# Kernel optimization log

Hardware: AMD Instinct MI355X
Metric: run time of the kernel (lower is better)

The kernel has to match this reference:

```python
import jax, jax.numpy as jnp
import numpy as np

B, N, F, K, NK, MID = 64, 100, 2048, 16, 8, 1024


def setup_inputs() -> dict:
    key = jax.random.key(0)
    ks = jax.random.split(key, 10)
    v = jax.random.normal(ks[0], (B, N, F), dtype=jnp.float32)
    v_mask = jnp.ones((B, N), dtype=jnp.float32)
    coord = jax.random.normal(ks[1], (B, N, N, 2), dtype=jnp.float32)
    adj_matrix = jax.random.uniform(ks[2], (B, N, K), dtype=jnp.float32)
    top_ind = jax.random.randint(ks[3], (B, N, K), 0, N)
    mean_rho = jax.random.uniform(ks[4], (NK,), minval=0.0, maxval=1.0)
    mean_theta = jax.random.uniform(ks[5], (NK,), minval=-np.pi, maxval=np.pi)
    precision_rho = jax.random.uniform(ks[6], (NK,), minval=0.0, maxval=1.0)
    precision_theta = jax.random.uniform(ks[7], (NK,), minval=0.0, maxval=1.0)
    # stacked per-kernel Linear weights: [NK, MID//NK, F] (no bias)
    W = jax.random.normal(ks[8], (NK, MID // NK, F), dtype=jnp.float32) * 0.02
    return {"v": v, "v_mask": v_mask, "coord": coord, "adj_matrix": adj_matrix,
            "top_ind": top_ind, "mean_rho": mean_rho, "mean_theta": mean_theta,
            "precision_rho": precision_rho, "precision_theta": precision_theta, "W": W}


def _gaussian_weights(coord, mean_rho, mean_theta, precision_rho, precision_theta):
    # coord: [B, N, N, 2] -> weights [B, N, N, NK], normalized over kernel axis
    rho = coord[..., 0][..., None]    # [B,N,N,1]
    theta = coord[..., 1][..., None]  # [B,N,N,1]
    w_rho = jnp.exp(-0.5 * (rho - mean_rho) ** 2 / (1e-14 + precision_rho ** 2))
    first_angle = jnp.abs(theta - mean_theta)
    second_angle = jnp.abs(2.0 * np.pi - first_angle)
    w_theta = jnp.exp(-0.5 * jnp.minimum(first_angle, second_angle) ** 2
                      / (1e-14 + precision_theta ** 2))
    w = w_rho * w_theta
    w = jnp.where(jnp.isnan(w), 0.0, w)
    # torch code normalizes the (-1, NK) view over dim=1 == kernel axis
    return w / (jnp.sum(w, axis=-1, keepdims=True) + 1e-14)


def reference(v, v_mask, coord, adj_matrix, top_ind,
              mean_rho, mean_theta, precision_rho, precision_theta, W):
    coord_weight = _gaussian_weights(coord, mean_rho, mean_theta,
                                     precision_rho, precision_theta)  # [B,N,N,NK]
    # gather top-K neighbor features: sparse_v[b,i,k] = v[b, top_ind[b,i,k]]
    sparse_v = jax.vmap(lambda vb, idx: vb[idx])(v, top_ind)           # [B,N,K,F]
    # gather corresponding Gaussian weights along neighbor axis
    sparse_weight = jnp.take_along_axis(coord_weight, top_ind[..., None], axis=2)  # [B,N,K,NK]
    attentive_v = sparse_v * adj_matrix[..., None]                     # weight_adj=True
    # weighted_neighbourhood = sparse_weight^T @ attentive_v : [B,N,NK,F]
    wn = jnp.einsum('bnkm,bnkf->bnmf', sparse_weight, attentive_v)
    # per-kernel linear then concat over kernels -> [B,N,NK*(MID//NK)]
    out = jnp.einsum('bnmf,mof->bnmo', wn, W)
    return out.reshape(v.shape[0], v.shape[1], -1)
```

## Files before the change

kernel.cpp:

```cpp
#include <hip/hip_runtime.h>
#include <math.h>

#define Bc 64
#define Nc 100
#define Fc 2048
#define Kc 16
#define NKc 8
#define BN (Bc*Nc)
#define MO 1024
#define TWO_PI 6.283185307179586f

typedef __attribute__((ext_vector_type(8))) short bf16x8;
typedef __attribute__((ext_vector_type(4))) float f32x4;

__device__ __forceinline__ unsigned short f2bf(float x) {
    union { float f; unsigned u; } c; c.f = x;
    unsigned r = c.u + 0x7FFFu + ((c.u >> 16) & 1u);
    return (unsigned short)(r >> 16);
}
__device__ __forceinline__ float bf2f(unsigned short x) {
    return __uint_as_float((unsigned)x << 16);
}

__global__ __launch_bounds__(256) void cvt_both(
    const float* __restrict__ v, const float* __restrict__ W,
    unsigned short* __restrict__ dst, int n8v, int n8tot)
{
    for (int i = blockIdx.x * blockDim.x + threadIdx.x; i < n8tot;
         i += gridDim.x * blockDim.x) {
        const float* src = (i < n8v) ? (v + (size_t)i * 8)
                                     : (W + (size_t)(i - n8v) * 8);
        const float4 x0 = ((const float4*)src)[0];
        const float4 x1 = ((const float4*)src)[1];
        bf16x8 o;
        o[0]=(short)f2bf(x0.x); o[1]=(short)f2bf(x0.y);
        o[2]=(short)f2bf(x0.z); o[3]=(short)f2bf(x0.w);
        o[4]=(short)f2bf(x1.x); o[5]=(short)f2bf(x1.y);
        o[6]=(short)f2bf(x1.z); o[7]=(short)f2bf(x1.w);
        *(bf16x8*)(dst + (size_t)i * 8) = o;
    }
}

__global__ __launch_bounds__(128) void weights_k(
    const float* __restrict__ coord, const float* __restrict__ adj,
    const int* __restrict__ top_ind,
    const float* __restrict__ mean_rho, const float* __restrict__ mean_theta,
    const float* __restrict__ prec_rho, const float* __restrict__ prec_theta,
    float* __restrict__ aw)
{
    __shared__ int   idx[Kc];
    __shared__ float wv[Kc][NKc];
    __shared__ float sc[Kc];
    const int bn = blockIdx.x;
    const int tid = threadIdx.x;
    if (tid < Kc) idx[tid] = top_ind[bn * Kc + tid];
    __syncthreads();
    const int k = tid >> 3, m = tid & 7;
    const int j = idx[k];
    const float rho   = coord[((size_t)bn * Nc + j) * 2 + 0];
    const float theta = coord[((size_t)bn * Nc + j) * 2 + 1];
    const float dr = rho - mean_rho[m];
    const float pr = prec_rho[m];
    const float wr = expf(-0.5f * dr * dr / (1e-14f + pr * pr));
    const float fa = fabsf(theta - mean_theta[m]);
    const float sa = fabsf(TWO_PI - fa);
    const float da = fminf(fa, sa);
    const float pt = prec_theta[m];
    const float wt = expf(-0.5f * da * da / (1e-14f + pt * pt));
    float w = wr * wt;
    if (w != w) w = 0.0f;
    wv[k][m] = w;
    __syncthreads();
    if (tid < Kc) {
        float s = 0.f;
        #pragma unroll
        for (int mm = 0; mm < NKc; ++mm) s += wv[tid][mm];
        sc[tid] = adj[bn * Kc + tid] / (s + 1e-14f);
    }
    __syncthreads();
    aw[(size_t)bn * 128 + m * 16 + k] = wv[k][m] * sc[k];
}

#define GBM 112
#define GBN 128
#define GBK 64
#define NT (Fc/GBK)
#define A_OFF   0
#define A_BUF   14336
#define B_OFF   28672
#define B_BUF   16384
#define IDX_OFF 30720
#define AW_OFF  37120

#define SYNC() do { asm volatile("s_waitcnt vmcnt(0)" ::: "memory"); \
                    __builtin_amdgcn_s_barrier(); \
                    __builtin_amdgcn_sched_barrier(0); } while (0)

template<int MI>
__device__ __forceinline__ void compute_tile(
    f32x4 (&acc)[4][4], const unsigned char* smem,
    int buf, int wm, int wn, int fr, int kg, int rsw)
{
    #pragma unroll
    for (int kk = 0; kk < 2; ++kk) {
        bf16x8 af[MI], bfr[4];
        #pragma unroll
        for (int mi = 0; mi < MI; ++mi)
            af[mi] = *(const bf16x8*)(smem + A_OFF + buf * A_BUF
                        + (wm * 64 + mi * 16 + fr) * 128
                        + ((kk * 32 + kg) ^ rsw) * 2);
        #pragma unroll
        for (int ni = 0; ni < 4; ++ni)
            bfr[ni] = *(const bf16x8*)(smem + B_OFF + buf * B_BUF
                        + (wn * 64 + ni * 16 + fr) * 128
                        + ((kk * 32 + kg) ^ rsw) * 2);
        #pragma unroll
        for (int mi = 0; mi < MI; ++mi)
            #pragma unroll
            for (int ni = 0; ni < 4; ++ni)
                acc[mi][ni] = __builtin_amdgcn_mfma_f32_16x16x32_bf16(
                    af[mi], bfr[ni], acc[mi][ni], 0, 0, 0);
    }
}

__global__ __launch_bounds__(256) void gemm_fused(
    const unsigned short* __restrict__ A,
    const unsigned short* __restrict__ B,
    const float* __restrict__ aw,
    const int* __restrict__ top_ind,
    float* __restrict__ out)
{
    __shared__ __align__(16) unsigned char smem[61440];

    const int tid = threadIdx.x;
    const int w  = tid >> 6, l = tid & 63;
    const int wm = w & 1,  wn = w >> 1;
    const int bid = blockIdx.x;
    const int b  = bid >> 3;
    const int jt = bid & 7;
    const int i0 = b * Nc;
    const int j0 = jt * GBN;

    const int srow = tid >> 3;
    const int scol = 8 * ((l & 7) ^ (l >> 3));

    const int fr = l & 15;
    const int kg = (l >> 4) * 8;
    const int rsw = 8 * (fr & 7);

    f32x4 acc[4][4] = {};

    auto stage = [&](int buf, int t) {
        const size_t k0 = (size_t)t * GBK;
        #pragma unroll
        for (int q = 0; q < 4; ++q) {
            const int row = q * 32 + srow;
            __builtin_amdgcn_global_load_lds(
                (const __attribute__((address_space(1))) void*)
                    (B + (size_t)(j0 + row) * Fc + k0 + scol),
                (__attribute__((address_space(3))) void*)
                    (smem + B_OFF + buf * B_BUF + q * 4096 + w * 1024),
                16, 0, 0);
        }
        #pragma unroll
        for (int q = 0; q < 3; ++q) {
            const int row = i0 + q * 32 + srow;
            __builtin_amdgcn_global_load_lds(
                (const __attribute__((address_space(1))) void*)
                    (A + (size_t)row * Fc + k0 + scol),
                (__attribute__((address_space(3))) void*)
                    (smem + A_OFF + buf * A_BUF + q * 4096 + w * 1024),
                16, 0, 0);
        }
        if (tid < 128) {
            int row = i0 + 96 + srow;
            if (row > BN - 1) row = BN - 1;
            __builtin_amdgcn_global_load_lds(
                (const __attribute__((address_space(1))) void*)
                    (A + (size_t)row * Fc + k0 + scol),
                (__attribute__((address_space(3))) void*)
                    (smem + A_OFF + buf * A_BUF + 3 * 4096 + w * 1024),
                16, 0, 0);
        }
    };

    #define COMPUTE(buf) do { \
        if (wm == 0) compute_tile<4>(acc, smem, (buf), wm, wn, fr, kg, rsw); \
        else         compute_tile<3>(acc, smem, (buf), wm, wn, fr, kg, rsw); \
    } while (0)

    stage(0, 0);
    SYNC();
    int t = 0;
    for (; t + 2 < NT; t += 2) {
        stage(1, t + 1);  COMPUTE(0);  SYNC();
        stage(0, t + 2);  COMPUTE(1);  SYNC();
    }
    stage(1, NT - 1);  COMPUTE(0);  SYNC();
    COMPUTE(1);

    __syncthreads();
    const int cn = l & 15;
    const int cr = (l >> 4) * 4;
    const int MIw = 4 - wm;
    #pragma unroll
    for (int mi = 0; mi < 4; ++mi) {
        if (mi < MIw) {
            #pragma unroll
            for (int ni = 0; ni < 4; ++ni) {
                #pragma unroll
                for (int r = 0; r < 4; ++r) {
                    const int row = wm * 64 + mi * 16 + cr + r;
                    const int col = wn * 64 + ni * 16 + cn;
                    *(unsigned short*)(smem + row * 264 + col * 2) =
                        f2bf(acc[mi][ni][r]);
                }
            }
        }
    }
    for (int i = tid; i < Nc * Kc; i += 256) {
        ((int*)(smem + IDX_OFF))[i] = top_ind[(size_t)b * Nc * Kc + i];
        ((float*)(smem + AW_OFF))[i] =
            aw[(size_t)(b * Nc + (i >> 4)) * 128 + jt * 16 + (i & 15)];
    }
    __syncthreads();

    const int cq = tid & 31;
    for (int n = tid >> 5; n < Nc; n += 8) {
        float4 o = make_float4(0.f, 0.f, 0.f, 0.f);
        #pragma unroll
        for (int k = 0; k < Kc; ++k) {
            const int   r = ((const int*)(smem + IDX_OFF))[n * Kc + k];
            const float a = ((const float*)(smem + AW_OFF))[n * Kc + k];
            const ushort4 u = *(const ushort4*)(smem + r * 264 + cq * 8);
            o.x += a * bf2f(u.x); o.y += a * bf2f(u.y);
            o.z += a * bf2f(u.z); o.w += a * bf2f(u.w);
        }
        *(float4*)&out[(size_t)(b * Nc + n) * MO + j0 + cq * 4] = o;
    }
}

#define TM 64
#define TN 64
#define FBK 16

__device__ __forceinline__ void compute_a(
    int bn, int tid,
    const float* __restrict__ coord, const float* __restrict__ adj,
    const int* __restrict__ top_ind,
    const float* __restrict__ mean_rho, const float* __restrict__ mean_theta,
    const float* __restrict__ prec_rho, const float* __restrict__ prec_theta,
    int (&lds_idx)[Kc], float (&lds_a)[Kc][NKc], float (&lds_scale)[Kc])
{
    if (tid < Kc) lds_idx[tid] = top_ind[bn * Kc + tid];
    __syncthreads();
    if (tid < Kc * NKc) {
        const int k = tid >> 3, m = tid & 7;
        const int j = lds_idx[k];
        const float rho   = coord[((size_t)bn * Nc + j) * 2 + 0];
        const float theta = coord[((size_t)bn * Nc + j) * 2 + 1];
        const float dr = rho - mean_rho[m];
        const float pr = prec_rho[m];
        const float wr = expf(-0.5f * dr * dr / (1e-14f + pr * pr));
        const float fa = fabsf(theta - mean_theta[m]);
        const float sa = fabsf(TWO_PI - fa);
        const float da = fminf(fa, sa);
        const float pt = prec_theta[m];
        const float wt = expf(-0.5f * da * da / (1e-14f + pt * pt));
        float w = wr * wt;
        if (w != w) w = 0.0f;
        lds_a[k][m] = w;
    }
    __syncthreads();
    if (tid < Kc) {
        float s = 0.f;
        #pragma unroll
        for (int m = 0; m < NKc; ++m) s += lds_a[tid][m];
        lds_scale[tid] = adj[bn * Kc + tid] / (s + 1e-14f);
    }
    __syncthreads();
    if (tid < Kc * NKc) {
        const int k = tid >> 3, m = tid & 7;
        lds_a[k][m] *= lds_scale[k];
    }
    __syncthreads();
}

__global__ __launch_bounds__(256) void gemm_p(
    const float* __restrict__ A,
    const float* __restrict__ Bm,
    float* __restrict__ P)
{
    __shared__ float At[FBK][TM + 4];
    __shared__ float Bt[FBK][TN + 4];
    const int tid = threadIdx.x;
    const int tx = tid & 15;
    const int ty = tid >> 4;
    const int i0 = blockIdx.x * TM;
    const int j0 = blockIdx.y * TN;
    const int lk = tid & 15;
    const int lr = tid >> 4;

    float acc[4][4] = {};

    for (int k0 = 0; k0 < Fc; k0 += FBK) {
        #pragma unroll
        for (int rr = 0; rr < 4; ++rr) {
            At[lk][lr + rr * 16] = A[(size_t)(i0 + lr + rr * 16) * Fc + k0 + lk];
            Bt[lk][lr + rr * 16] = Bm[(size_t)(j0 + lr + rr * 16) * Fc + k0 + lk];
        }
        __syncthreads();
        #pragma unroll
        for (int kk = 0; kk < FBK; ++kk) {
            float a4[4], b4[4];
            #pragma unroll
            for (int p = 0; p < 4; ++p) a4[p] = At[kk][ty * 4 + p];
            #pragma unroll
            for (int p = 0; p < 4; ++p) b4[p] = Bt[kk][tx * 4 + p];
            #pragma unroll
            for (int pi = 0; pi < 4; ++pi)
                #pragma unroll
                for (int pj = 0; pj < 4; ++pj)
                    acc[pi][pj] += a4[pi] * b4[pj];
        }
        __syncthreads();
    }

    #pragma unroll
    for (int pi = 0; pi < 4; ++pi)
        #pragma unroll
        for (int pj = 0; pj < 4; ++pj)
            P[(size_t)(i0 + ty * 4 + pi) * MO + j0 + tx * 4 + pj] = acc[pi][pj];
}

__global__ __launch_bounds__(256) void combine_f32(
    const float* __restrict__ P,
    const float* __restrict__ coord, const float* __restrict__ adj,
    const int* __restrict__ top_ind,
    const float* __restrict__ mr, const float* __restrict__ mt,
    const float* __restrict__ pr, const float* __restrict__ pt,
    float* __restrict__ out)
{
    __shared__ int   lds_idx[Kc];
    __shared__ float lds_a[Kc][NKc];
    __shared__ float lds_scale[Kc];
    const int bn = blockIdx.x;
    const int tid = threadIdx.x;
    const int b = bn / Nc;

    compute_a(bn, tid, coord, adj, top_ind, mr, mt, pr, pt,
              lds_idx, lds_a, lds_scale);

    const int m = tid >> 5;
    float ak[Kc];
    size_t rowoff[Kc];
    #pragma unroll
    for (int k = 0; k < Kc; ++k) {
        ak[k] = lds_a[k][m];
        rowoff[k] = (size_t)(b * Nc + lds_idx[k]) * MO + tid * 4;
    }
    float4 acc = make_float4(0.f, 0.f, 0.f, 0.f);
    #pragma unroll
    for (int k = 0; k < Kc; ++k) {
        const float4 p = *(const float4*)&P[rowoff[k]];
        acc.x += ak[k] * p.x; acc.y += ak[k] * p.y;
        acc.z += ak[k] * p.z; acc.w += ak[k] * p.w;
    }
    *(float4*)&out[(size_t)bn * MO + tid * 4] = acc;
}

extern "C" void kernel_launch(void* const* d_in, const int* in_sizes, int n_in,
                              void* d_out, int out_size, void* d_ws, size_t ws_size,
                              hipStream_t stream) {
    const float* v        = (const float*)d_in[0];
    const float* coord    = (const float*)d_in[2];
    const float* adj      = (const float*)d_in[3];
    const int*   top_ind  = (const int*)d_in[4];
    const float* mr       = (const float*)d_in[5];
    const float* mt       = (const float*)d_in[6];
    const float* pr       = (const float*)d_in[7];
    const float* pt       = (const float*)d_in[8];
    const float* W        = (const float*)d_in[9];
    float* out = (float*)d_out;

    const size_t vbBytes = (size_t)BN * Fc * sizeof(unsigned short);
    const size_t WbBytes = (size_t)MO * Fc * sizeof(unsigned short);
    const size_t awBytes = (size_t)BN * 128 * sizeof(float);
    const size_t needBF  = vbBytes + WbBytes + awBytes;
    const size_t PBytes  = (size_t)BN * MO * sizeof(float);

    if (ws_size >= needBF) {
        char* ws = (char*)d_ws;
        unsigned short* vb = (unsigned short*)ws;
        unsigned short* Wb = vb + (size_t)BN * Fc;
        float* aw          = (float*)(ws + vbBytes + WbBytes);

        const int n8v   = BN * Fc / 8;
        const int n8tot = n8v + MO * Fc / 8;
        cvt_both<<<7424, 256, 0, stream>>>(v, W, vb, n8v, n8tot);

        weights_k<<<BN, 128, 0, stream>>>(coord, adj, top_ind,
                                          mr, mt, pr, pt, aw);

        gemm_fused<<<512, 256, 0, stream>>>(vb, Wb, aw, top_ind, out);
    } else if (ws_size >= PBytes) {
        float* P = (float*)d_ws;
        gemm_p<<<dim3(BN / TM, MO / TN), 256, 0, stream>>>(v, W, P);
        combine_f32<<<BN, 256, 0, stream>>>(P, coord, adj, top_ind,
                                            mr, mt, pr, pt, out);
    }
}
```

Baseline: 65.75 us.

## Merge conversion and weight kernels into one launch; remap GEMM blocks per XCD

The bf16 conversion kernel and the Gaussian weight kernel are fused into a single prep launch. Block ranges are split by role: the first blocks convert one chunk each with no grid-stride loop, and the remaining blocks compute weights for two rows each. This removes one kernel launch and the gap between the two kernels. The GEMM block index is also remapped so that the blocks of one batch land on the same XCD, which should improve L2 reuse of that batch's A rows. The cost is a larger conversion grid and role divergence inside the prep kernel.

```diff
diff --git a/kernel.cpp b/kernel.cpp
--- a/kernel.cpp
+++ b/kernel.cpp
@@ -22,12 +22,19 @@
     return __uint_as_float((unsigned)x << 16);
 }
 
-__global__ __launch_bounds__(256) void cvt_both(
+__global__ __launch_bounds__(256) void prep(
     const float* __restrict__ v, const float* __restrict__ W,
-    unsigned short* __restrict__ dst, int n8v, int n8tot)
-{
-    for (int i = blockIdx.x * blockDim.x + threadIdx.x; i < n8tot;
-         i += gridDim.x * blockDim.x) {
+    unsigned short* __restrict__ dst, int n8v, int nCvt,
+    const float* __restrict__ coord, const float* __restrict__ adj,
+    const int* __restrict__ top_ind,
+    const float* __restrict__ mean_rho, const float* __restrict__ mean_theta,
+    const float* __restrict__ prec_rho, const float* __restrict__ prec_theta,
+    float* __restrict__ aw)
+{
+    const int bid = blockIdx.x;
+    const int tid = threadIdx.x;
+    if (bid < nCvt) {
+        const int i = bid * 256 + tid;
         const float* src = (i < n8v) ? (v + (size_t)i * 8)
                                      : (W + (size_t)(i - n8v) * 8);
         const float4 x0 = ((const float4*)src)[0];
@@ -38,25 +45,18 @@
         o[4]=(short)f2bf(x1.x); o[5]=(short)f2bf(x1.y);
         o[6]=(short)f2bf(x1.z); o[7]=(short)f2bf(x1.w);
         *(bf16x8*)(dst + (size_t)i * 8) = o;
-    }
-}
-
-__global__ __launch_bounds__(128) void weights_k(
-    const float* __restrict__ coord, const float* __restrict__ adj,
-    const int* __restrict__ top_ind,
-    const float* __restrict__ mean_rho, const float* __restrict__ mean_theta,
-    const float* __restrict__ prec_rho, const float* __restrict__ prec_theta,
-    float* __restrict__ aw)
-{
-    __shared__ int   idx[Kc];
-    __shared__ float wv[Kc][NKc];
-    __shared__ float sc[Kc];
-    const int bn = blockIdx.x;
-    const int tid = threadIdx.x;
-    if (tid < Kc) idx[tid] = top_ind[bn * Kc + tid];
-    __syncthreads();
-    const int k = tid >> 3, m = tid & 7;
-    const int j = idx[k];
+        return;
+    }
+    __shared__ int   idx[2][Kc];
+    __shared__ float wv[2][Kc][NKc];
+    __shared__ float sc[2][Kc];
+    const int h  = tid >> 7;
+    const int t7 = tid & 127;
+    const int bn = (bid - nCvt) * 2 + h;
+    if (t7 < Kc) idx[h][t7] = top_ind[bn * Kc + t7];
+    __syncthreads();
+    const int k = t7 >> 3, m = t7 & 7;
+    const int j = idx[h][k];
     const float rho   = coord[((size_t)bn * Nc + j) * 2 + 0];
     const float theta = coord[((size_t)bn * Nc + j) * 2 + 1];
     const float dr = rho - mean_rho[m];
@@ -69,16 +69,16 @@
     const float wt = expf(-0.5f * da * da / (1e-14f + pt * pt));
     float w = wr * wt;
     if (w != w) w = 0.0f;
-    wv[k][m] = w;
-    __syncthreads();
-    if (tid < Kc) {
+    wv[h][k][m] = w;
+    __syncthreads();
+    if (t7 < Kc) {
         float s = 0.f;
         #pragma unroll
-        for (int mm = 0; mm < NKc; ++mm) s += wv[tid][mm];
-        sc[tid] = adj[bn * Kc + tid] / (s + 1e-14f);
-    }
-    __syncthreads();
-    aw[(size_t)bn * 128 + m * 16 + k] = wv[k][m] * sc[k];
+        for (int mm = 0; mm < NKc; ++mm) s += wv[h][t7][mm];
+        sc[h][t7] = adj[bn * Kc + t7] / (s + 1e-14f);
+    }
+    __syncthreads();
+    aw[(size_t)bn * 128 + m * 16 + k] = wv[h][k][m] * sc[h][k];
 }
 
 #define GBM 112
@@ -136,8 +136,10 @@
     const int w  = tid >> 6, l = tid & 63;
     const int wm = w & 1,  wn = w >> 1;
     const int bid = blockIdx.x;
-    const int b  = bid >> 3;
-    const int jt = bid & 7;
+    const int xcd  = bid & 7;
+    const int slot = bid >> 3;
+    const int b  = xcd * 8 + (slot >> 3);
+    const int jt = slot & 7;
     const int i0 = b * Nc;
     const int j0 = jt * GBN;
 
@@ -396,11 +398,11 @@
         float* aw          = (float*)(ws + vbBytes + WbBytes);
 
         const int n8v   = BN * Fc / 8;
-        const int n8tot = n8v + MO * Fc / 8;
-        cvt_both<<<7424, 256, 0, stream>>>(v, W, vb, n8v, n8tot);
-
-        weights_k<<<BN, 128, 0, stream>>>(coord, adj, top_ind,
-                                          mr, mt, pr, pt, aw);
+        const int nCvt  = (n8v + MO * Fc / 8) / 256;
+        const int nWgt  = BN / 2;
+        prep<<<nCvt + nWgt, 256, 0, stream>>>(v, W, vb, n8v, nCvt,
+                                              coord, adj, top_ind,
+                                              mr, mt, pr, pt, aw);
 
         gemm_fused<<<512, 256, 0, stream>>>(vb, Wb, aw, top_ind, out);
     } else if (ws_size >= PBytes) {
```

After: 60.91 us. 7.4% less time.
